# Optimization experiments

Measured on AMD Instinct MI355X. Metric: run time of the kernel, lower is better.

Reference implementation:

```python
import jax, jax.numpy as jnp
import numpy as np

N_NODES = 100000
N_EDGES = 3200000


def _sage_conv(x, src, dst, Wl, Wr, b):
    # PyG SAGEConv (aggr='mean', root_weight=True, bias on lin_l):
    # out_i = mean_{j in N(i)} x_j @ Wl + x_i @ Wr + b
    msg = x[src]                                            # [E, F] gather
    s = jax.ops.segment_sum(msg, dst, num_segments=N_NODES)  # [N, F]
    cnt = jax.ops.segment_sum(jnp.ones((src.shape[0], 1), x.dtype), dst,
                              num_segments=N_NODES)          # [N, 1]
    agg = s / jnp.maximum(cnt, 1.0)                          # mean (0 for isolated nodes)
    return agg @ Wl + x @ Wr + b


def setup_inputs() -> dict:
    key = jax.random.key(0)
    ks = jax.random.split(key, 12)
    in_d, hid, out_d = 32, 24, 12
    x = jax.random.normal(ks[0], (N_NODES, in_d), dtype=jnp.float32)
    edge_index = jax.random.randint(ks[1], (2, N_EDGES), 0, N_NODES, dtype=jnp.int64)

    def glorot(k, fan_in, fan_out):
        lim = np.sqrt(6.0 / (fan_in + fan_out)).astype(np.float32)
        return jax.random.uniform(k, (fan_in, fan_out), jnp.float32, -lim, lim)

    return {
        "x": x,
        "edge_index": edge_index,
        "Wl1": glorot(ks[2], in_d, hid), "Wr1": glorot(ks[3], in_d, hid),
        "b1": jnp.zeros((hid,), jnp.float32),
        "Wl2": glorot(ks[4], hid, hid), "Wr2": glorot(ks[5], hid, hid),
        "b2": jnp.zeros((hid,), jnp.float32),
        "Wl3": glorot(ks[6], hid, out_d), "Wr3": glorot(ks[7], hid, out_d),
        "b3": jnp.zeros((out_d,), jnp.float32),
    }


def reference(x, edge_index, Wl1, Wr1, b1, Wl2, Wr2, b2, Wl3, Wr3, b3):
    src, dst = edge_index[0], edge_index[1]
    h = jax.nn.relu(_sage_conv(x, src, dst, Wl1, Wr1, b1))
    h = jax.nn.relu(_sage_conv(h, src, dst, Wl2, Wr2, b2))
    h = jax.nn.sigmoid(_sage_conv(h, src, dst, Wl3, Wr3, b3))
    return h
```

## Files before the change

### kernel.cpp

```cpp
#include <hip/hip_runtime.h>
#include <cstdint>
#include <cstddef>

#define NT 256
constexpr int SHIFT  = 7;
constexpr int NBK    = 1024;
constexpr int BMASK  = (1 << SHIFT) - 1;
constexpr int EPB    = 12800;
constexpr int TSPLIT = 50000;
constexpr int STCAP  = 6144;

__device__ __forceinline__ float sigf(float v) {
    return 1.0f / (1.0f + __expf(-v));
}
__device__ __forceinline__ float bf2f(unsigned short u) {
    return __uint_as_float((unsigned)u << 16);
}
__device__ __forceinline__ unsigned short f2bf(float f) {
    unsigned u = __float_as_uint(f);
    return (unsigned short)((u + 0x7fffu + ((u >> 16) & 1u)) >> 16);
}

__global__ __launch_bounds__(NT)
void part_k(const int* __restrict__ src, const int* __restrict__ dst,
            unsigned* __restrict__ part, int* __restrict__ runstart,
            int* __restrict__ runcnt, int* __restrict__ totcnt,
            int e_total, int nPB)
{
    __shared__ unsigned stage[EPB];
    __shared__ int hist[NBK];
    __shared__ int curs[NBK];
    __shared__ int tsum[NT];
    const int b    = blockIdx.x;
    const int t    = threadIdx.x;
    const int base = b * EPB;
    const int nh   = min(EPB, e_total - base);

    for (int i = t; i < NBK; i += NT) hist[i] = 0;
    __syncthreads();
    for (int i = t; i < nh; i += NT)
        atomicAdd(&hist[dst[base + i] >> SHIFT], 1);
    __syncthreads();

    const int f0 = 4 * t;
    int h0 = hist[f0], h1 = hist[f0 + 1], h2 = hist[f0 + 2], h3 = hist[f0 + 3];
    int incl = h0 + h1 + h2 + h3;
    tsum[t] = incl;
    __syncthreads();
    for (int off = 1; off < NT; off <<= 1) {
        int add = (t >= off) ? tsum[t - off] : 0;
        __syncthreads();
        tsum[t] += add;
        __syncthreads();
    }
    int ex = tsum[t] - incl;
    curs[f0]     = ex;
    curs[f0 + 1] = ex + h0;
    curs[f0 + 2] = ex + h0 + h1;
    curs[f0 + 3] = ex + h0 + h1 + h2;
    runstart[(f0    ) * nPB + b] = base + ex;
    runstart[(f0 + 1) * nPB + b] = base + ex + h0;
    runstart[(f0 + 2) * nPB + b] = base + ex + h0 + h1;
    runstart[(f0 + 3) * nPB + b] = base + ex + h0 + h1 + h2;
    runcnt[(f0    ) * nPB + b] = h0;
    runcnt[(f0 + 1) * nPB + b] = h1;
    runcnt[(f0 + 2) * nPB + b] = h2;
    runcnt[(f0 + 3) * nPB + b] = h3;
    if (h0) atomicAdd(&totcnt[f0],     h0);
    if (h1) atomicAdd(&totcnt[f0 + 1], h1);
    if (h2) atomicAdd(&totcnt[f0 + 2], h2);
    if (h3) atomicAdd(&totcnt[f0 + 3], h3);
    __syncthreads();

    for (int i = t; i < nh; i += NT) {
        int d = dst[base + i];
        int s = src[base + i];
        int f = d >> SHIFT;
        int r = atomicAdd(&curs[f], 1);
        stage[r] = ((unsigned)s << SHIFT) | (unsigned)(d & BMASK);
    }
    __syncthreads();

    for (int i = t; i < nh; i += NT) part[base + i] = stage[i];
}

__global__ __launch_bounds__(1024)
void tscan_k(const int* __restrict__ totcnt, int* __restrict__ fbase)
{
    __shared__ int s[1024];
    int t = threadIdx.x;
    int v = totcnt[t];
    s[t] = v;
    __syncthreads();
    for (int off = 1; off < 1024; off <<= 1) {
        int add = (t >= off) ? s[t - off] : 0;
        __syncthreads();
        s[t] += add;
        __syncthreads();
    }
    fbase[t] = s[t] - v;
}

__global__ __launch_bounds__(NT)
void b_k(const unsigned* __restrict__ part, const int* __restrict__ runstart,
         const int* __restrict__ runcnt, const int* __restrict__ fbase,
         int* __restrict__ row_ptr, int* __restrict__ mptr,
         int* __restrict__ col, int nPB, int n)
{
    constexpr int NB2 = 1 << SHIFT;
    __shared__ unsigned stage[STCAP];
    __shared__ int rss[NT], rcs[NT], lof[NT], ssum[NT];
    __shared__ int d0[NB2], dt[NB2], sc[NB2], c0[NB2], c1[NB2];
    const int f = blockIdx.x;
    const int t = threadIdx.x;

    int rc = 0, rs = 0;
    if (t < nPB) { rs = runstart[f * nPB + t]; rc = runcnt[f * nPB + t]; }
    rss[t] = rs;
    rcs[t] = rc;
    ssum[t] = rc;
    __syncthreads();
    for (int off = 1; off < NT; off <<= 1) {
        int add = (t >= off) ? ssum[t - off] : 0;
        __syncthreads();
        ssum[t] += add;
        __syncthreads();
    }
    lof[t] = ssum[t] - rc;
    __syncthreads();
    const int tot = ssum[NT - 1];

    if (t < NB2) { d0[t] = 0; dt[t] = 0; }
    __syncthreads();

    if (tot <= STCAP) {
        const int lane = t & 15;
        const int rg   = t >> 4;
        for (int chunk = 0; chunk < nPB; chunk += 16) {
            int r = chunk + rg;
            if (r < nPB) {
                int s0 = rss[r], c = rcs[r], lo = lof[r];
                for (int i = lane; i < c; i += 16)
                    stage[lo + i] = part[s0 + i];
            }
        }
        __syncthreads();
        for (int i = t; i < tot; i += NT) {
            unsigned p = stage[i];
            int l = p & BMASK;
            atomicAdd(&dt[l], 1);
            if ((int)(p >> SHIFT) < TSPLIT) atomicAdd(&d0[l], 1);
        }
    } else {
        for (int i = 0; i < rc; ++i) {
            unsigned p = part[rs + i];
            int l = p & BMASK;
            atomicAdd(&dt[l], 1);
            if ((int)(p >> SHIFT) < TSPLIT) atomicAdd(&d0[l], 1);
        }
    }
    __syncthreads();

    if (t < NB2) sc[t] = dt[t];
    __syncthreads();
    for (int off = 1; off < NB2; off <<= 1) {
        int add = (t >= off && t < NB2) ? sc[t - off] : 0;
        __syncthreads();
        if (t < NB2) sc[t] += add;
        __syncthreads();
    }
    if (t < NB2) {
        int excl = sc[t] - dt[t];
        int st0  = fbase[f] + excl;
        int node = (f << SHIFT) + t;
        if (node <= n) row_ptr[node] = st0;
        if (node <  n) mptr[node]    = st0 + d0[t];
        c0[t] = st0;
        c1[t] = st0 + d0[t];
    }
    __syncthreads();

    if (tot <= STCAP) {
        for (int i = t; i < tot; i += NT) {
            unsigned p = stage[i];
            int l = p & BMASK;
            int s = (int)(p >> SHIFT);
            int pos = atomicAdd((s < TSPLIT) ? &c0[l] : &c1[l], 1);
            col[pos] = s;
        }
    } else {
        for (int i = 0; i < rc; ++i) {
            unsigned p = part[rs + i];
            int l = p & BMASK;
            int s = (int)(p >> SHIFT);
            int pos = atomicAdd((s < TSPLIT) ? &c0[l] : &c1[l], 1);
            col[pos] = s;
        }
    }
}

__global__ __launch_bounds__(NT)
void cvt_k(const float* __restrict__ x, unsigned short* __restrict__ xb, int ntot)
{
    int i = blockIdx.x * NT + threadIdx.x;
    if (i < ntot) xb[i] = f2bf(x[i]);
}

__global__ __launch_bounds__(NT)
void gA_k(const unsigned short* __restrict__ Hin, const int* __restrict__ row_ptr,
          const int* __restrict__ mptr, const int* __restrict__ col,
          float* __restrict__ P, int n)
{
    const int lane8 = threadIdx.x & 7;
    const int grp   = threadIdx.x >> 3;
    const int node  = blockIdx.x * (NT / 8) + grp;
    if (node >= n) return;
    const int e0 = row_ptr[node];
    const int e1 = mptr[node];
    const ushort4* rows = reinterpret_cast<const ushort4*>(Hin);
    float a0 = 0.f, a1 = 0.f, a2 = 0.f, a3 = 0.f;
    int e = e0;
    for (; e + 3 < e1; e += 4) {
        int s0 = col[e], s1 = col[e + 1], s2 = col[e + 2], s3 = col[e + 3];
        ushort4 v0 = rows[(size_t)s0 * 8 + lane8];
        ushort4 v1 = rows[(size_t)s1 * 8 + lane8];
        ushort4 v2 = rows[(size_t)s2 * 8 + lane8];
        ushort4 v3 = rows[(size_t)s3 * 8 + lane8];
        a0 += bf2f(v0.x) + bf2f(v1.x) + bf2f(v2.x) + bf2f(v3.x);
        a1 += bf2f(v0.y) + bf2f(v1.y) + bf2f(v2.y) + bf2f(v3.y);
        a2 += bf2f(v0.z) + bf2f(v1.z) + bf2f(v2.z) + bf2f(v3.z);
        a3 += bf2f(v0.w) + bf2f(v1.w) + bf2f(v2.w) + bf2f(v3.w);
    }
    for (; e < e1; ++e) {
        ushort4 v0 = rows[(size_t)col[e] * 8 + lane8];
        a0 += bf2f(v0.x); a1 += bf2f(v0.y); a2 += bf2f(v0.z); a3 += bf2f(v0.w);
    }
    reinterpret_cast<float4*>(P + (size_t)node * 32)[lane8] = make_float4(a0, a1, a2, a3);
}

template<int FIN, int FOUT, int ACT>
__global__ __launch_bounds__(NT)
void gB_k(const unsigned short* __restrict__ Hin, const int* __restrict__ row_ptr,
          const int* __restrict__ mptr, const int* __restrict__ col,
          const float* __restrict__ P, const float* __restrict__ Wl,
          const float* __restrict__ Wr, const float* __restrict__ b,
          void* __restrict__ Hout, int n)
{
    constexpr int FS  = 32;
    constexpr int NPB = NT / 8;
    constexpr int GS  = 2 * FS + 4;
    __shared__ float sm[NPB * GS];

    const int lane8 = threadIdx.x & 7;
    const int grp   = threadIdx.x >> 3;
    const int node  = blockIdx.x * NPB + grp;
    const bool valid = node < n;

    if (valid) {
        const int rp0 = row_ptr[node];
        const int rpm = mptr[node];
        const int rp1 = row_ptr[node + 1];
        const ushort4* rows = reinterpret_cast<const ushort4*>(Hin);
        float4 pv = reinterpret_cast<const float4*>(P + (size_t)node * 32)[lane8];
        float a0 = pv.x, a1 = pv.y, a2 = pv.z, a3 = pv.w;
        ushort4 xv = rows[(size_t)node * 8 + lane8];
        int e = rpm;
        for (; e + 3 < rp1; e += 4) {
            int s0 = col[e], s1 = col[e + 1], s2 = col[e + 2], s3 = col[e + 3];
            ushort4 v0 = rows[(size_t)s0 * 8 + lane8];
            ushort4 v1 = rows[(size_t)s1 * 8 + lane8];
            ushort4 v2 = rows[(size_t)s2 * 8 + lane8];
            ushort4 v3 = rows[(size_t)s3 * 8 + lane8];
            a0 += bf2f(v0.x) + bf2f(v1.x) + bf2f(v2.x) + bf2f(v3.x);
            a1 += bf2f(v0.y) + bf2f(v1.y) + bf2f(v2.y) + bf2f(v3.y);
            a2 += bf2f(v0.z) + bf2f(v1.z) + bf2f(v2.z) + bf2f(v3.z);
            a3 += bf2f(v0.w) + bf2f(v1.w) + bf2f(v2.w) + bf2f(v3.w);
        }
        for (; e < rp1; ++e) {
            ushort4 v0 = rows[(size_t)col[e] * 8 + lane8];
            a0 += bf2f(v0.x); a1 += bf2f(v0.y); a2 += bf2f(v0.z); a3 += bf2f(v0.w);
        }
        float invd = 1.0f / fmaxf((float)(rp1 - rp0), 1.0f);
        float* smg = sm + grp * GS;
        smg[4 * lane8 + 0]      = a0 * invd;
        smg[4 * lane8 + 1]      = a1 * invd;
        smg[4 * lane8 + 2]      = a2 * invd;
        smg[4 * lane8 + 3]      = a3 * invd;
        smg[FS + 4 * lane8 + 0] = bf2f(xv.x);
        smg[FS + 4 * lane8 + 1] = bf2f(xv.y);
        smg[FS + 4 * lane8 + 2] = bf2f(xv.z);
        smg[FS + 4 * lane8 + 3] = bf2f(xv.w);
    }
    __syncthreads();

    if (!valid) return;
    const float* smg = sm + grp * GS;

    if constexpr (ACT == 0) {
        unsigned short* out = (unsigned short*)Hout + (size_t)node * FS;
#pragma unroll
        for (int j = 0; j < 4; ++j) {
            int f = lane8 + 8 * j;
            float r = 0.0f;
            if (f < FOUT) {
                float a = b[f];
#pragma unroll
                for (int k = 0; k < FIN; ++k) {
                    a = fmaf(smg[k],      Wl[k * FOUT + f], a);
                    a = fmaf(smg[FS + k], Wr[k * FOUT + f], a);
                }
                r = fmaxf(a, 0.0f);
            }
            out[f] = f2bf(r);
        }
    } else {
        float* out = (float*)Hout + (size_t)node * FOUT;
#pragma unroll
        for (int j = 0; j < (FOUT + 7) / 8; ++j) {
            int f = lane8 + 8 * j;
            if (f < FOUT) {
                float a = b[f];
#pragma unroll
                for (int k = 0; k < FIN; ++k) {
                    a = fmaf(smg[k],      Wl[k * FOUT + f], a);
                    a = fmaf(smg[FS + k], Wr[k * FOUT + f], a);
                }
                out[f] = sigf(a);
            }
        }
    }
}

extern "C" void kernel_launch(void* const* d_in, const int* in_sizes, int n_in,
                              void* d_out, int out_size, void* d_ws, size_t ws_size,
                              hipStream_t stream)
{
    const float* x   = (const float*)d_in[0];
    const int*   ei  = (const int*)d_in[1];
    const float* Wl1 = (const float*)d_in[2];
    const float* Wr1 = (const float*)d_in[3];
    const float* b1  = (const float*)d_in[4];
    const float* Wl2 = (const float*)d_in[5];
    const float* Wr2 = (const float*)d_in[6];
    const float* b2  = (const float*)d_in[7];
    const float* Wl3 = (const float*)d_in[8];
    const float* Wr3 = (const float*)d_in[9];
    const float* b3  = (const float*)d_in[10];

    const int N = in_sizes[0] / 32;
    const int E = in_sizes[1] / 2;
    const int* src = ei;
    const int* dst = ei + E;

    const int nPB = (E + EPB - 1) / EPB;
    const int nBK = ((N - 1) >> SHIFT) + 1;
    const int nbG = (N + 31) / 32;
    const int nbC = (N * 32 + NT - 1) / NT;

    int* runstart = (int*)d_ws;
    int* runcnt   = runstart + (size_t)NBK * nPB;
    int* totcnt   = runcnt + (size_t)NBK * nPB;
    int* fbase    = totcnt + 1024;
    int* row_ptr  = fbase + 1024;
    int* mptr     = row_ptr + (N + 2);
    size_t off    = 2 * (size_t)NBK * nPB + 2048 + (N + 2) + N;
    off = (off + 3) & ~(size_t)3;
    int* col      = (int*)d_ws + off;
    off += E;
    unsigned* part = (unsigned*)((int*)d_ws + off);
    float*    P    = (float*)part;
    off += E;
    unsigned short* xb  = (unsigned short*)((int*)d_ws + off);
    unsigned short* H1b = xb  + (size_t)N * 32;
    unsigned short* H2b = H1b + (size_t)N * 32;

    hipMemsetAsync(totcnt, 0, 1024 * sizeof(int), stream);

    part_k <<<nPB, NT,   0, stream>>>(src, dst, part, runstart, runcnt, totcnt, E, nPB);
    tscan_k<<<1,   1024, 0, stream>>>(totcnt, fbase);
    b_k    <<<nBK, NT,   0, stream>>>(part, runstart, runcnt, fbase, row_ptr, mptr, col, nPB, N);

    cvt_k  <<<nbC, NT,   0, stream>>>(x, xb, N * 32);

    gA_k            <<<nbG, NT, 0, stream>>>(xb,  row_ptr, mptr, col, P, N);
    gB_k<32, 24, 0> <<<nbG, NT, 0, stream>>>(xb,  row_ptr, mptr, col, P, Wl1, Wr1, b1, H1b, N);
    gA_k            <<<nbG, NT, 0, stream>>>(H1b, row_ptr, mptr, col, P, N);
    gB_k<24, 24, 0> <<<nbG, NT, 0, stream>>>(H1b, row_ptr, mptr, col, P, Wl2, Wr2, b2, H2b, N);
    gA_k            <<<nbG, NT, 0, stream>>>(H2b, row_ptr, mptr, col, P, N);
    gB_k<24, 12, 1> <<<nbG, NT, 0, stream>>>(H2b, row_ptr, mptr, col, P, Wl3, Wr3, b3, (float*)d_out, N);
}
```

Before: 281.0 us.

## Sort nodes by degree for balanced gather blocks and halve partition chunk size

Adds a degree histogram, scan and scatter pass that builds a degree-sorted node permutation. The gather kernels process nodes through this permutation so each warp handles nodes of similar degree, which reduces lane divergence in the edge loops. Separately, halves edges per partition block and lets b_k handle up to 512 runs per bucket. The cost is three extra small kernels, an indirection load per node, and scattered P and output accesses in node order.

```diff
diff --git a/kernel.cpp b/kernel.cpp
--- a/kernel.cpp
+++ b/kernel.cpp
@@ -6,7 +6,8 @@
 constexpr int SHIFT  = 7;
 constexpr int NBK    = 1024;
 constexpr int BMASK  = (1 << SHIFT) - 1;
-constexpr int EPB    = 12800;
+constexpr int EPB    = 6400;
+constexpr int NPR    = 512;
 constexpr int TSPLIT = 50000;
 constexpr int STCAP  = 6144;
 
@@ -109,16 +110,21 @@
 {
     constexpr int NB2 = 1 << SHIFT;
     __shared__ unsigned stage[STCAP];
-    __shared__ int rss[NT], rcs[NT], lof[NT], ssum[NT];
+    __shared__ int rss[NPR], rcs[NPR], lof[NPR];
+    __shared__ int ssum[NT];
     __shared__ int d0[NB2], dt[NB2], sc[NB2], c0[NB2], c1[NB2];
     const int f = blockIdx.x;
     const int t = threadIdx.x;
 
-    int rc = 0, rs = 0;
-    if (t < nPB) { rs = runstart[f * nPB + t]; rc = runcnt[f * nPB + t]; }
-    rss[t] = rs;
-    rcs[t] = rc;
-    ssum[t] = rc;
+    const int l0 = 2 * t, l1 = 2 * t + 1;
+    int rc0 = (l0 < nPB) ? runcnt[f * nPB + l0] : 0;
+    int rc1 = (l1 < nPB) ? runcnt[f * nPB + l1] : 0;
+    rss[l0] = (l0 < nPB) ? runstart[f * nPB + l0] : 0;
+    rss[l1] = (l1 < nPB) ? runstart[f * nPB + l1] : 0;
+    rcs[l0] = rc0;
+    rcs[l1] = rc1;
+    int incl = rc0 + rc1;
+    ssum[t] = incl;
     __syncthreads();
     for (int off = 1; off < NT; off <<= 1) {
         int add = (t >= off) ? ssum[t - off] : 0;
@@ -126,7 +132,9 @@
         ssum[t] += add;
         __syncthreads();
     }
-    lof[t] = ssum[t] - rc;
+    int ex = ssum[t] - incl;
+    lof[l0] = ex;
+    lof[l1] = ex + rc0;
     __syncthreads();
     const int tot = ssum[NT - 1];
 
@@ -134,13 +142,13 @@
     __syncthreads();
 
     if (tot <= STCAP) {
-        const int lane = t & 15;
-        const int rg   = t >> 4;
-        for (int chunk = 0; chunk < nPB; chunk += 16) {
+        const int lane = t & 7;
+        const int rg   = t >> 3;
+        for (int chunk = 0; chunk < nPB; chunk += 32) {
             int r = chunk + rg;
             if (r < nPB) {
                 int s0 = rss[r], c = rcs[r], lo = lof[r];
-                for (int i = lane; i < c; i += 16)
+                for (int i = lane; i < c; i += 8)
                     stage[lo + i] = part[s0 + i];
             }
         }
@@ -152,11 +160,14 @@
             if ((int)(p >> SHIFT) < TSPLIT) atomicAdd(&d0[l], 1);
         }
     } else {
-        for (int i = 0; i < rc; ++i) {
-            unsigned p = part[rs + i];
-            int l = p & BMASK;
-            atomicAdd(&dt[l], 1);
-            if ((int)(p >> SHIFT) < TSPLIT) atomicAdd(&d0[l], 1);
+        for (int r = t; r < nPB; r += NT) {
+            int s0 = rss[r], c = rcs[r];
+            for (int i = 0; i < c; ++i) {
+                unsigned p = part[s0 + i];
+                int l = p & BMASK;
+                atomicAdd(&dt[l], 1);
+                if ((int)(p >> SHIFT) < TSPLIT) atomicAdd(&d0[l], 1);
+            }
         }
     }
     __syncthreads();
@@ -189,13 +200,60 @@
             col[pos] = s;
         }
     } else {
-        for (int i = 0; i < rc; ++i) {
-            unsigned p = part[rs + i];
-            int l = p & BMASK;
-            int s = (int)(p >> SHIFT);
-            int pos = atomicAdd((s < TSPLIT) ? &c0[l] : &c1[l], 1);
-            col[pos] = s;
-        }
+        for (int r = t; r < nPB; r += NT) {
+            int s0 = rss[r], c = rcs[r];
+            for (int i = 0; i < c; ++i) {
+                unsigned p = part[s0 + i];
+                int l = p & BMASK;
+                int s = (int)(p >> SHIFT);
+                int pos = atomicAdd((s < TSPLIT) ? &c0[l] : &c1[l], 1);
+                col[pos] = s;
+            }
+        }
+    }
+}
+
+__global__ __launch_bounds__(NT)
+void dh_k(const int* __restrict__ row_ptr, int* __restrict__ dbin, int n)
+{
+    __shared__ int h[128];
+    if (threadIdx.x < 128) h[threadIdx.x] = 0;
+    __syncthreads();
+    int i = blockIdx.x * NT + threadIdx.x;
+    if (i < n) {
+        int deg = min(row_ptr[i + 1] - row_ptr[i], 127);
+        atomicAdd(&h[deg], 1);
+    }
+    __syncthreads();
+    if (threadIdx.x < 128 && h[threadIdx.x])
+        atomicAdd(&dbin[threadIdx.x], h[threadIdx.x]);
+}
+
+__global__ __launch_bounds__(128)
+void dscan_k(const int* __restrict__ dbin, int* __restrict__ dcur)
+{
+    __shared__ int s[128];
+    int t = threadIdx.x;
+    int v = dbin[t];
+    s[t] = v;
+    __syncthreads();
+    for (int off = 1; off < 128; off <<= 1) {
+        int add = (t >= off) ? s[t - off] : 0;
+        __syncthreads();
+        s[t] += add;
+        __syncthreads();
+    }
+    dcur[t] = s[t] - v;
+}
+
+__global__ __launch_bounds__(NT)
+void df_k(const int* __restrict__ row_ptr, int* dcur, int* __restrict__ perm, int n)
+{
+    int i = blockIdx.x * NT + threadIdx.x;
+    if (i < n) {
+        int deg = min(row_ptr[i + 1] - row_ptr[i], 127);
+        int pos = atomicAdd(&dcur[deg], 1);
+        perm[pos] = i;
     }
 }
 
@@ -209,12 +267,13 @@
 __global__ __launch_bounds__(NT)
 void gA_k(const unsigned short* __restrict__ Hin, const int* __restrict__ row_ptr,
           const int* __restrict__ mptr, const int* __restrict__ col,
-          float* __restrict__ P, int n)
+          const int* __restrict__ perm, float* __restrict__ P, int n)
 {
     const int lane8 = threadIdx.x & 7;
     const int grp   = threadIdx.x >> 3;
-    const int node  = blockIdx.x * (NT / 8) + grp;
-    if (node >= n) return;
+    const int gid   = blockIdx.x * (NT / 8) + grp;
+    if (gid >= n) return;
+    const int node  = perm[gid];
     const int e0 = row_ptr[node];
     const int e1 = mptr[node];
     const ushort4* rows = reinterpret_cast<const ushort4*>(Hin);
@@ -242,9 +301,9 @@
 __global__ __launch_bounds__(NT)
 void gB_k(const unsigned short* __restrict__ Hin, const int* __restrict__ row_ptr,
           const int* __restrict__ mptr, const int* __restrict__ col,
-          const float* __restrict__ P, const float* __restrict__ Wl,
-          const float* __restrict__ Wr, const float* __restrict__ b,
-          void* __restrict__ Hout, int n)
+          const int* __restrict__ perm, const float* __restrict__ P,
+          const float* __restrict__ Wl, const float* __restrict__ Wr,
+          const float* __restrict__ b, void* __restrict__ Hout, int n)
 {
     constexpr int FS  = 32;
     constexpr int NPB = NT / 8;
@@ -253,8 +312,9 @@
 
     const int lane8 = threadIdx.x & 7;
     const int grp   = threadIdx.x >> 3;
-    const int node  = blockIdx.x * NPB + grp;
-    const bool valid = node < n;
+    const int gid   = blockIdx.x * NPB + grp;
+    const bool valid = gid < n;
+    const int node  = valid ? perm[gid] : 0;
 
     if (valid) {
         const int rp0 = row_ptr[node];
@@ -355,15 +415,19 @@
     const int nPB = (E + EPB - 1) / EPB;
     const int nBK = ((N - 1) >> SHIFT) + 1;
     const int nbG = (N + 31) / 32;
+    const int nbN = (N + NT - 1) / NT;
     const int nbC = (N * 32 + NT - 1) / NT;
 
     int* runstart = (int*)d_ws;
     int* runcnt   = runstart + (size_t)NBK * nPB;
     int* totcnt   = runcnt + (size_t)NBK * nPB;
-    int* fbase    = totcnt + 1024;
-    int* row_ptr  = fbase + 1024;
+    int* dbin     = totcnt + 1024;
+    int* fbase    = dbin + 128;
+    int* dcur     = fbase + 1024;
+    int* row_ptr  = dcur + 128;
     int* mptr     = row_ptr + (N + 2);
-    size_t off    = 2 * (size_t)NBK * nPB + 2048 + (N + 2) + N;
+    int* perm     = mptr + N;
+    size_t off    = 2 * (size_t)NBK * nPB + 2304 + (N + 2) + 2 * (size_t)N;
     off = (off + 3) & ~(size_t)3;
     int* col      = (int*)d_ws + off;
     off += E;
@@ -374,18 +438,22 @@
     unsigned short* H1b = xb  + (size_t)N * 32;
     unsigned short* H2b = H1b + (size_t)N * 32;
 
-    hipMemsetAsync(totcnt, 0, 1024 * sizeof(int), stream);
+    hipMemsetAsync(totcnt, 0, (1024 + 128) * sizeof(int), stream);
 
     part_k <<<nPB, NT,   0, stream>>>(src, dst, part, runstart, runcnt, totcnt, E, nPB);
     tscan_k<<<1,   1024, 0, stream>>>(totcnt, fbase);
     b_k    <<<nBK, NT,   0, stream>>>(part, runstart, runcnt, fbase, row_ptr, mptr, col, nPB, N);
 
+    dh_k   <<<nbN, NT,   0, stream>>>(row_ptr, dbin, N);
+    dscan_k<<<1,   128,  0, stream>>>(dbin, dcur);
+    df_k   <<<nbN, NT,   0, stream>>>(row_ptr, dcur, perm, N);
+
     cvt_k  <<<nbC, NT,   0, stream>>>(x, xb, N * 32);
 
-    gA_k            <<<nbG, NT, 0, stream>>>(xb,  row_ptr, mptr, col, P, N);
-    gB_k<32, 24, 0> <<<nbG, NT, 0, stream>>>(xb,  row_ptr, mptr, col, P, Wl1, Wr1, b1, H1b, N);
-    gA_k            <<<nbG, NT, 0, stream>>>(H1b, row_ptr, mptr, col, P, N);
-    gB_k<24, 24, 0> <<<nbG, NT, 0, stream>>>(H1b, row_ptr, mptr, col, P, Wl2, Wr2, b2, H2b, N);
-    gA_k            <<<nbG, NT, 0, stream>>>(H2b, row_ptr, mptr, col, P, N);
-    gB_k<24, 12, 1> <<<nbG, NT, 0, stream>>>(H2b, row_ptr, mptr, col, P, Wl3, Wr3, b3, (float*)d_out, N);
-}
+    gA_k            <<<nbG, NT, 0, stream>>>(xb,  row_ptr, mptr, col, perm, P, N);
+    gB_k<32, 24, 0> <<<nbG, NT, 0, stream>>>(xb,  row_ptr, mptr, col, perm, P, Wl1, Wr1, b1, H1b, N);
+    gA_k            <<<nbG, NT, 0, stream>>>(H1b, row_ptr, mptr, col, perm, P, N);
+    gB_k<24, 24, 0> <<<nbG, NT, 0, stream>>>(H1b, row_ptr, mptr, col, perm, P, Wl2, Wr2, b2, H2b, N);
+    gA_k            <<<nbG, NT, 0, stream>>>(H2b, row_ptr, mptr, col, perm, P, N);
+    gB_k<24, 12, 1> <<<nbG, NT, 0, stream>>>(H2b, row_ptr, mptr, col, perm, P, Wl3, Wr3, b3, (float*)d_out, N);
+}
```

Result: slower. 503.7 us (+79.3%).
